# Kernel tuning notes

Measured on AMD Instinct MI355X. Metric: run time of the kernel, lower is better.

## Reference

```python
import jax, jax.numpy as jnp
from jax import lax
import numpy as np

D_MODEL = 1024
D_STATE = 16
D_CONV = 4
EXPAND = 2
D_INNER = EXPAND * D_MODEL  # 2048
DT_RANK = D_MODEL // 16     # 64
EPS = 1e-5


def _ln(x, g, b):
    mu = jnp.mean(x, axis=-1, keepdims=True)
    var = jnp.mean(jnp.square(x - mu), axis=-1, keepdims=True)
    return (x - mu) * lax.rsqrt(var + EPS) * g + b


def setup_inputs() -> dict:
    key = jax.random.key(0)
    ks = jax.random.split(key, 16)
    B, L = 2, 1024
    s = 0.02  # weight init scale
    inp = {
        'x': jax.random.normal(ks[0], (B, L, D_MODEL), jnp.float32),
        'n1_g': jnp.ones((D_MODEL,), jnp.float32),
        'n1_b': jnp.zeros((D_MODEL,), jnp.float32),
        'n2_g': jnp.ones((D_MODEL,), jnp.float32),
        'n2_b': jnp.zeros((D_MODEL,), jnp.float32),
        'in_proj_w': jax.random.normal(ks[1], (2 * D_INNER, D_MODEL), jnp.float32) * s,
        'conv_w': jax.random.normal(ks[2], (D_INNER, 1, D_CONV), jnp.float32) * 0.1,
        'conv_b': jnp.zeros((D_INNER,), jnp.float32),
        'x_proj_w': jax.random.normal(ks[3], (DT_RANK + 2 * D_STATE, D_INNER), jnp.float32) * s,
        'dt_w': jax.random.normal(ks[4], (D_INNER, DT_RANK), jnp.float32) * s,
        'dt_b': jnp.full((D_INNER,), -4.0, jnp.float32) + jax.random.normal(ks[5], (D_INNER,), jnp.float32) * 0.1,
        'A_log': jnp.tile(jnp.log(jnp.arange(1, D_STATE + 1, dtype=jnp.float32))[None, :], (D_INNER, 1)),
        'D': jnp.ones((D_INNER,), jnp.float32),
        'out_w': jax.random.normal(ks[6], (D_MODEL, D_INNER), jnp.float32) * s,
        'ffg_w': jax.random.normal(ks[7], (2 * D_MODEL, D_MODEL), jnp.float32) * s,
        'ffg_b': jnp.zeros((2 * D_MODEL,), jnp.float32),
        'ffp_w': jax.random.normal(ks[8], (D_MODEL, D_MODEL), jnp.float32) * s,
        'ffp_b': jnp.zeros((D_MODEL,), jnp.float32),
    }
    return inp


def _mamba(u, in_proj_w, conv_w, conv_b, x_proj_w, dt_w, dt_b, A_log, D, out_w):
    Bsz, L, _ = u.shape
    xz = u @ in_proj_w.T                      # [B,L,2*Di]
    x_in, z = jnp.split(xz, 2, axis=-1)
    # depthwise causal conv over time
    xc = x_in.transpose(0, 2, 1)              # [B,Di,L]
    xc = lax.conv_general_dilated(
        xc, conv_w, window_strides=(1,), padding=[(D_CONV - 1, 0)],
        dimension_numbers=('NCH', 'OIH', 'NCH'), feature_group_count=D_INNER)
    xc = jax.nn.silu(xc + conv_b[None, :, None]).transpose(0, 2, 1)  # [B,L,Di]
    # input-dependent SSM params
    x_dbl = xc @ x_proj_w.T                   # [B,L,dt_rank+2*N]
    dt, Bm, Cm = jnp.split(x_dbl, [DT_RANK, DT_RANK + D_STATE], axis=-1)
    delta = jax.nn.softplus(dt @ dt_w.T + dt_b)        # [B,L,Di]
    A = -jnp.exp(A_log)                                # [Di,N]
    dA = jnp.exp(jnp.einsum('bld,dn->bldn', delta, A))   # [B,L,Di,N]
    dBu = jnp.einsum('bld,bln,bld->bldn', delta, Bm, xc)  # [B,L,Di,N]

    def step(h, inp):
        dA_t, dBu_t, C_t = inp
        h = dA_t * h + dBu_t                  # [B,Di,N]
        y = jnp.einsum('bdn,bn->bd', h, C_t)
        return h, y

    h0 = jnp.zeros((Bsz, D_INNER, D_STATE), u.dtype)
    _, ys = lax.scan(step, h0, (dA.transpose(1, 0, 2, 3),
                                dBu.transpose(1, 0, 2, 3),
                                Cm.transpose(1, 0, 2)))
    y = ys.transpose(1, 0, 2) + xc * D        # skip via D
    y = y * jax.nn.silu(z)                    # output gate
    return y @ out_w.T


def reference(x, n1_g, n1_b, n2_g, n2_b, in_proj_w, conv_w, conv_b, x_proj_w,
              dt_w, dt_b, A_log, D, out_w, ffg_w, ffg_b, ffp_w, ffp_b):
    # x = x + ssm(norm1(x))
    x = x + _mamba(_ln(x, n1_g, n1_b), in_proj_w, conv_w, conv_b, x_proj_w,
                   dt_w, dt_b, A_log, D, out_w)
    # gated FFN residual
    normed = _ln(x, n2_g, n2_b)
    gate, val = jnp.split(normed @ ffg_w.T + ffg_b, 2, axis=-1)
    x = x + (jax.nn.silu(gate) * val) @ ffp_w.T + ffp_b
    return x
```

## Files before the change

kernel.cpp:

```cpp
#include <hip/hip_runtime.h>
#include <hip/hip_bf16.h>

#define DM 1024
#define DI 2048
#define LSEQ 1024
#define BSZ 2
#define NROWS (BSZ*LSEQ)
#define NC 32
#define CL 32

typedef __attribute__((ext_vector_type(4))) float f32x4;
typedef __attribute__((ext_vector_type(8))) short bf16x8;
typedef __hip_bfloat16 bf16;

__device__ __forceinline__ float sigmoidf_(float x){ return 1.f/(1.f+__expf(-x)); }

__global__ void cvt_kernel(const float* __restrict__ src, bf16* __restrict__ dst,
                           long n, int cols, int src_stride, int src_rows)
{
  long i = (long)blockIdx.x*blockDim.x + threadIdx.x;
  if (i >= n) return;
  int r = (int)(i / cols);
  int c = (int)(i - (long)r*cols);
  float v = (r < src_rows) ? src[(long)r*src_stride + c] : 0.f;
  dst[i] = __float2bfloat16(v);
}

__global__ __launch_bounds__(256) void ln_kernel(const float* __restrict__ x,
    const float* __restrict__ g, const float* __restrict__ b, bf16* __restrict__ out)
{
  int row = blockIdx.x;
  float4 v = ((const float4*)(x + (long)row*DM))[threadIdx.x];
  float s  = v.x+v.y+v.z+v.w;
  float s2 = v.x*v.x+v.y*v.y+v.z*v.z+v.w*v.w;
  #pragma unroll
  for (int m=32;m;m>>=1){ s += __shfl_xor(s,m); s2 += __shfl_xor(s2,m); }
  __shared__ float ws0[4], ws1[4];
  int wv = threadIdx.x>>6;
  if ((threadIdx.x&63)==0){ ws0[wv]=s; ws1[wv]=s2; }
  __syncthreads();
  s  = ws0[0]+ws0[1]+ws0[2]+ws0[3];
  s2 = ws1[0]+ws1[1]+ws1[2]+ws1[3];
  float mu  = s*(1.f/DM);
  float var = s2*(1.f/DM) - mu*mu;
  float rs  = rsqrtf(var + 1e-5f);
  int c = threadIdx.x*4;
  float4 gg = ((const float4*)g)[threadIdx.x];
  float4 bb = ((const float4*)b)[threadIdx.x];
  bf16* o = out + (long)row*DM + c;
  o[0] = __float2bfloat16((v.x-mu)*rs*gg.x + bb.x);
  o[1] = __float2bfloat16((v.y-mu)*rs*gg.y + bb.y);
  o[2] = __float2bfloat16((v.z-mu)*rs*gg.z + bb.z);
  o[3] = __float2bfloat16((v.w-mu)*rs*gg.w + bb.w);
}

template<int ACT>
__global__ __launch_bounds__(256)
void gemm_k(const short* __restrict__ A, int lda, const short* __restrict__ B, int ldb,
            int K, int Nreal, int ldo, int pstride,
            const float* __restrict__ bias, const float* __restrict__ res,
            float* __restrict__ outf, bf16* __restrict__ outb)
{
  A += (size_t)blockIdx.z * K;
  B += (size_t)blockIdx.z * K;
  if (outf) outf += (size_t)blockIdx.z * pstride;

  __shared__ short As[2][128*32];
  __shared__ short Bs[2][128*32];
  const int tid  = threadIdx.x;
  const int wave = tid>>6, lane = tid&63;
  const int m0 = blockIdx.x*128, n0 = blockIdx.y*128;
  const int wm = (wave>>1)*64, wn = (wave&1)*64;
  const int lr = lane&15, lk = lane>>4;

  f32x4 acc[4][4];
  #pragma unroll
  for (int i=0;i<4;i++)
    #pragma unroll
    for (int j=0;j<4;j++) acc[i][j] = f32x4{0.f,0.f,0.f,0.f};

  const int r0 = tid>>2;
  const int kb = (tid&3)*8;
  const short* Arow = A + (size_t)(m0+r0)*lda + kb;
  const short* Brow = B + (size_t)(n0+r0)*ldb + kb;

#define STAGE_T(buf, kt) do { \
    __builtin_amdgcn_global_load_lds((const __attribute__((address_space(1))) void*)(Arow + (kt)), \
        (__attribute__((address_space(3))) void*)(&As[buf][r0*32+kb]), 16, 0, 0); \
    __builtin_amdgcn_global_load_lds((const __attribute__((address_space(1))) void*)(Arow + (size_t)64*lda + (kt)), \
        (__attribute__((address_space(3))) void*)(&As[buf][(r0+64)*32+kb]), 16, 0, 0); \
    __builtin_amdgcn_global_load_lds((const __attribute__((address_space(1))) void*)(Brow + (kt)), \
        (__attribute__((address_space(3))) void*)(&Bs[buf][r0*32+kb]), 16, 0, 0); \
    __builtin_amdgcn_global_load_lds((const __attribute__((address_space(1))) void*)(Brow + (size_t)64*ldb + (kt)), \
        (__attribute__((address_space(3))) void*)(&Bs[buf][(r0+64)*32+kb]), 16, 0, 0); \
  } while(0)

  STAGE_T(0, 0);
  asm volatile("s_waitcnt vmcnt(0)");
  __syncthreads();
  int cur = 0;
  for (int kt = 32; kt <= K; kt += 32) {
    if (kt < K) STAGE_T(cur^1, kt);
    bf16x8 af[4], bfr[4];
    #pragma unroll
    for (int i=0;i<4;i++) af[i]  = *(const bf16x8*)(&As[cur][(wm+i*16+lr)*32 + lk*8]);
    #pragma unroll
    for (int j=0;j<4;j++) bfr[j] = *(const bf16x8*)(&Bs[cur][(wn+j*16+lr)*32 + lk*8]);
    #pragma unroll
    for (int i=0;i<4;i++)
      #pragma unroll
      for (int j=0;j<4;j++)
        acc[i][j] = __builtin_amdgcn_mfma_f32_16x16x32_bf16(af[i], bfr[j], acc[i][j], 0,0,0);
    asm volatile("s_waitcnt vmcnt(0)");
    __syncthreads();
    cur ^= 1;
  }
#undef STAGE_T

  #pragma unroll
  for (int i=0;i<4;i++){
    #pragma unroll
    for (int j=0;j<4;j++){
      int col = n0 + wn + j*16 + lr;
      if (col >= Nreal) continue;
      #pragma unroll
      for (int r=0;r<4;r++){
        int row = m0 + wm + i*16 + lk*4 + r;
        float v = acc[i][j][r];
        if (bias) v += bias[col];
        if (ACT==1){
          float ev = __expf(v);
          v = (v > 20.f) ? v : __logf(1.f + ev);
        }
        if (res)  v += res[(size_t)row*ldo + col];
        if (outf) outf[(size_t)row*ldo + col] = v;
        if (outb) outb[(size_t)row*ldo + col] = __float2bfloat16(v);
      }
    }
  }
}

__global__ __launch_bounds__(256) void red2_kernel(
    const float* __restrict__ p0, const float* __restrict__ p1,
    const float* __restrict__ bias, const float* __restrict__ res,
    float* __restrict__ outf)
{
  long i = ((long)blockIdx.x*256 + threadIdx.x)*4;
  float4 a = *(const float4*)(p0+i);
  float4 b = *(const float4*)(p1+i);
  float4 o = {a.x+b.x, a.y+b.y, a.z+b.z, a.w+b.w};
  if (bias){
    const float4 bb = *(const float4*)(bias + (int)(i & (DM-1)));
    o.x+=bb.x; o.y+=bb.y; o.z+=bb.z; o.w+=bb.w;
  }
  if (res){
    float4 r = *(const float4*)(res+i);
    o.x+=r.x; o.y+=r.y; o.z+=r.z; o.w+=r.w;
  }
  *(float4*)(outf+i) = o;
}

__global__ __launch_bounds__(256) void xproj_reduce(const float* __restrict__ part,
    float* __restrict__ xdbl, bf16* __restrict__ dt16)
{
  int i = blockIdx.x*256 + threadIdx.x;
  if (i >= NROWS*96) return;
  float s = 0.f;
  #pragma unroll
  for (int k=0;k<8;k++) s += part[(long)k*(NROWS*96) + i];
  xdbl[i] = s;
  int r = i/96, c = i - r*96;
  if (c < 64) dt16[r*64 + c] = __float2bfloat16(s);
}

__global__ __launch_bounds__(256) void conv_kernel(const bf16* __restrict__ xz,
    const float* __restrict__ w, const float* __restrict__ cb,
    float* __restrict__ xcf, bf16* __restrict__ xcb)
{
  long i = (long)blockIdx.x*blockDim.x + threadIdx.x;
  int d  = (int)(i & (DI-1));
  int bl = (int)(i >> 11);
  int l  = bl & (LSEQ-1);
  int b  = bl >> 10;
  float acc = cb[d];
  #pragma unroll
  for (int k=0;k<4;k++){
    int ls = l-3+k;
    if (ls >= 0)
      acc += __bfloat162float(xz[(long)(b*LSEQ+ls)*(2*DI) + d]) * w[d*4+k];
  }
  float s = acc * sigmoidf_(acc);
  xcf[i] = s;
  xcb[i] = __float2bfloat16(s);
}


#define H16(du, duxv, B0,B1,B2,B3) \
  h0  = __expf((du)*An0 )*h0  + (duxv)*(B0).x; \
  h1  = __expf((du)*An1 )*h1  + (duxv)*(B0).y; \
  h2  = __expf((du)*An2 )*h2  + (duxv)*(B0).z; \
  h3  = __expf((du)*An3 )*h3  + (duxv)*(B0).w; \
  h4  = __expf((du)*An4 )*h4  + (duxv)*(B1).x; \
  h5  = __expf((du)*An5 )*h5  + (duxv)*(B1).y; \
  h6  = __expf((du)*An6 )*h6  + (duxv)*(B1).z; \
  h7  = __expf((du)*An7 )*h7  + (duxv)*(B1).w; \
  h8  = __expf((du)*An8 )*h8  + (duxv)*(B2).x; \
  h9  = __expf((du)*An9 )*h9  + (duxv)*(B2).y; \
  h10 = __expf((du)*An10)*h10 + (duxv)*(B2).z; \
  h11 = __expf((du)*An11)*h11 + (duxv)*(B2).w; \
  h12 = __expf((du)*An12)*h12 + (duxv)*(B3).x; \
  h13 = __expf((du)*An13)*h13 + (duxv)*(B3).y; \
  h14 = __expf((du)*An14)*h14 + (duxv)*(B3).z; \
  h15 = __expf((du)*An15)*h15 + (duxv)*(B3).w;

#define DECL_AN(Alog_ptr, d) \
  float4 al0 = ((const float4*)((Alog_ptr) + (d)*16))[0]; \
  float4 al1 = ((const float4*)((Alog_ptr) + (d)*16))[1]; \
  float4 al2 = ((const float4*)((Alog_ptr) + (d)*16))[2]; \
  float4 al3 = ((const float4*)((Alog_ptr) + (d)*16))[3]; \
  float An0=-__expf(al0.x), An1=-__expf(al0.y), An2 =-__expf(al0.z), An3 =-__expf(al0.w); \
  float An4=-__expf(al1.x), An5=-__expf(al1.y), An6 =-__expf(al1.z), An7 =-__expf(al1.w); \
  float An8=-__expf(al2.x), An9=-__expf(al2.y), An10=-__expf(al2.z), An11=-__expf(al2.w); \
  float An12=-__expf(al3.x),An13=-__expf(al3.y),An14=-__expf(al3.z), An15=-__expf(al3.w);

__global__ __launch_bounds__(256) void scan_p1(
    const float* __restrict__ delta, const float* __restrict__ xc,
    const float* __restrict__ xdbl, const float* __restrict__ A_log,
    float* __restrict__ S, float* __restrict__ sumDu)
{
  const int tid = threadIdx.x;
  const int d   = blockIdx.x*256 + tid;
  const int c   = blockIdx.y, b = blockIdx.z;
  const int bd  = b*2048 + d;
  DECL_AN(A_log, d);
  __shared__ float sB[CL][16];
  {
    int e = tid*2;
    int r = e>>4, n = e&15;
    long row = (long)b*LSEQ + c*CL + r;
    sB[r][n]   = xdbl[row*96 + 64 + n];
    sB[r][n+1] = xdbl[row*96 + 64 + n+1];
  }
  __syncthreads();
  float h0=0,h1=0,h2=0,h3=0,h4=0,h5=0,h6=0,h7=0,
        h8=0,h9=0,h10=0,h11=0,h12=0,h13=0,h14=0,h15=0;
  float sdu = 0.f;
  const long rbase = (long)b*LSEQ + c*CL;
  #pragma unroll
  for (int s0=0; s0<CL; s0+=8){
    float du8[8], xv8[8];
    #pragma unroll
    for (int i=0;i<8;i++){
      long row = rbase + s0 + i;
      du8[i] = delta[row*DI + d];
      xv8[i] = xc[row*DI + d];
    }
    #pragma unroll
    for (int i=0;i<8;i++){
      float du = du8[i], duxv = du*xv8[i];
      sdu += du;
      const float4* bb = (const float4*)sB[s0+i];
      float4 B0=bb[0], B1=bb[1], B2=bb[2], B3=bb[3];
      H16(du, duxv, B0,B1,B2,B3);
    }
  }
  sumDu[c*4096 + bd] = sdu;
  float hs[16] = {h0,h1,h2,h3,h4,h5,h6,h7,h8,h9,h10,h11,h12,h13,h14,h15};
  #pragma unroll
  for (int n=0;n<16;n++) S[(c*16+n)*4096 + bd] = hs[n];
}

__global__ __launch_bounds__(256) void scan_p2(const float* __restrict__ S,
    const float* __restrict__ sumDu, const float* __restrict__ A_log,
    float* __restrict__ hin)
{
  int t = blockIdx.x*256 + threadIdx.x;
  int n = t >> 12, bd = t & 4095;
  int d = bd & 2047;
  float Aneg = -__expf(A_log[d*16 + n]);
  float h = 0.f;
  #pragma unroll
  for (int c=0;c<NC;c++){
    hin[(c*16+n)*4096 + bd] = h;
    float P = __expf(Aneg * sumDu[c*4096 + bd]);
    h = S[(c*16+n)*4096 + bd] + P*h;
  }
}

__global__ __launch_bounds__(256) void scan_p3(
    const float* __restrict__ delta, const float* __restrict__ xc,
    const float* __restrict__ xdbl, const bf16* __restrict__ xz,
    const float* __restrict__ A_log, const float* __restrict__ Dp,
    const float* __restrict__ hin, bf16* __restrict__ y)
{
  const int tid = threadIdx.x;
  const int d   = blockIdx.x*256 + tid;
  const int c   = blockIdx.y, b = blockIdx.z;
  const int bd  = b*2048 + d;
  DECL_AN(A_log, d);
  const float Dd = Dp[d];
  __shared__ float sB[CL][16], sC[CL][16];
  {
    int e = tid*2;
    int r = e>>4, n = e&15;
    long row = (long)b*LSEQ + c*CL + r;
    sB[r][n]   = xdbl[row*96 + 64 + n];
    sB[r][n+1] = xdbl[row*96 + 64 + n+1];
    sC[r][n]   = xdbl[row*96 + 80 + n];
    sC[r][n+1] = xdbl[row*96 + 80 + n+1];
  }
  __syncthreads();
  float h0,h1,h2,h3,h4,h5,h6,h7,h8,h9,h10,h11,h12,h13,h14,h15;
  {
    const float* hp = hin + c*16*4096 + bd;
    h0 =hp[0];       h1 =hp[4096];    h2 =hp[2*4096];  h3 =hp[3*4096];
    h4 =hp[4*4096];  h5 =hp[5*4096];  h6 =hp[6*4096];  h7 =hp[7*4096];
    h8 =hp[8*4096];  h9 =hp[9*4096];  h10=hp[10*4096]; h11=hp[11*4096];
    h12=hp[12*4096]; h13=hp[13*4096]; h14=hp[14*4096]; h15=hp[15*4096];
  }
  const long rbase = (long)b*LSEQ + c*CL;
  #pragma unroll
  for (int s0=0; s0<CL; s0+=8){
    float du8[8], xv8[8], zv8[8];
    #pragma unroll
    for (int i=0;i<8;i++){
      long row = rbase + s0 + i;
      du8[i] = delta[row*DI + d];
      xv8[i] = xc[row*DI + d];
      zv8[i] = __bfloat162float(xz[row*(2*DI) + DI + d]);
    }
    #pragma unroll
    for (int i=0;i<8;i++){
      float du = du8[i], xv = xv8[i], duxv = du*xv;
      const float4* bb = (const float4*)sB[s0+i];
      float4 B0=bb[0], B1=bb[1], B2=bb[2], B3=bb[3];
      H16(du, duxv, B0,B1,B2,B3);
      const float4* cc = (const float4*)sC[s0+i];
      float4 C0=cc[0], C1=cc[1], C2=cc[2], C3=cc[3];
      float r0 = h0*C0.x + h4*C1.x + h8 *C2.x + h12*C3.x;
      float r1 = h1*C0.y + h5*C1.y + h9 *C2.y + h13*C3.y;
      float r2 = h2*C0.z + h6*C1.z + h10*C2.z + h14*C3.z;
      float r3 = h3*C0.w + h7*C1.w + h11*C2.w + h15*C3.w;
      float r = (r0+r1) + (r2+r3) + xv*Dd;
      float z = zv8[i];
      y[(rbase+s0+i)*DI + d] = __float2bfloat16(r * (z*sigmoidf_(z)));
    }
  }
}

__global__ __launch_bounds__(256) void gated_kernel(const float* __restrict__ gv,
                                                    bf16* __restrict__ g)
{
  long i = (long)blockIdx.x*blockDim.x + threadIdx.x;
  int r = (int)(i >> 10);
  int c = (int)(i & (DM-1));
  float gt = gv[(long)r*(2*DM) + c];
  float vl = gv[(long)r*(2*DM) + DM + c];
  g[i] = __float2bfloat16(gt * sigmoidf_(gt) * vl);
}

extern "C" void kernel_launch(void* const* d_in, const int* in_sizes, int n_in,
                              void* d_out, int out_size, void* d_ws, size_t ws_size,
                              hipStream_t stream)
{
  const float* x        = (const float*)d_in[0];
  const float* n1_g     = (const float*)d_in[1];
  const float* n1_b     = (const float*)d_in[2];
  const float* n2_g     = (const float*)d_in[3];
  const float* n2_b     = (const float*)d_in[4];
  const float* in_proj_w= (const float*)d_in[5];
  const float* conv_w   = (const float*)d_in[6];
  const float* conv_b   = (const float*)d_in[7];
  const float* x_proj_w = (const float*)d_in[8];
  const float* dt_w     = (const float*)d_in[9];
  const float* dt_b     = (const float*)d_in[10];
  const float* A_log    = (const float*)d_in[11];
  const float* Dp       = (const float*)d_in[12];
  const float* out_w    = (const float*)d_in[13];
  const float* ffg_w    = (const float*)d_in[14];
  const float* ffg_b    = (const float*)d_in[15];
  const float* ffp_w    = (const float*)d_in[16];
  const float* ffp_b    = (const float*)d_in[17];

  char* ws = (char*)d_ws;
  bf16* w_inproj = (bf16*)(ws + 0);
  bf16* w_xproj  = (bf16*)(ws + 8388608);
  bf16* w_dt     = (bf16*)(ws + 8912896);
  bf16* w_out    = (bf16*)(ws + 9175040);
  bf16* w_ffg    = (bf16*)(ws + 13369344);
  bf16* w_ffp    = (bf16*)(ws + 17563648);
  bf16* x1_b     = (bf16*)(ws + 19660800);
  bf16* xz_b     = (bf16*)(ws + 23855104);
  float* part_fp = (float*)(ws + 23855104);
  bf16* xc_b     = (bf16*)(ws + 40632320);
  float* S_buf   = (float*)(ws + 40632320);
  float* sumDu   = (float*)(ws + 8388608);
  bf16* dt16     = (bf16*)(ws + 49020928);
  bf16* y_b      = (bf16*)(ws + 49283072);
  float* xc_f    = (float*)(ws + 57671680);
  float* xdbl_f  = (float*)(ws + 74448896);
  float* delta_f = (float*)(ws + 75235328);
  float* part_xp = (float*)(ws + 75235328);
  float* part_op = (float*)(ws + 75235328);
  float* x2_f    = (float*)(ws + 92012544);
  float* hin     = (float*)(ws + 92012544);
  float* outp    = (float*)d_out;

  #define GRID1(n) dim3((int)(((n)+255)/256))
  cvt_kernel<<<GRID1(4096L*1024), 256, 0, stream>>>(in_proj_w, w_inproj, 4096L*1024, 1024, 1024, 4096);
  cvt_kernel<<<GRID1(128L*2048), 256, 0, stream>>>(x_proj_w,  w_xproj,  128L*2048, 2048, 2048, 96);
  cvt_kernel<<<GRID1(2048L*64),  256, 0, stream>>>(dt_w,      w_dt,     2048L*64,   64,   64, 2048);
  cvt_kernel<<<GRID1(1024L*2048),256, 0, stream>>>(out_w,     w_out,    1024L*2048, 2048, 2048, 1024);
  cvt_kernel<<<GRID1(2048L*1024),256, 0, stream>>>(ffg_w,     w_ffg,    2048L*1024, 1024, 1024, 2048);
  cvt_kernel<<<GRID1(1024L*1024),256, 0, stream>>>(ffp_w,     w_ffp,    1024L*1024, 1024, 1024, 1024);

  ln_kernel<<<NROWS, 256, 0, stream>>>(x, n1_g, n1_b, x1_b);
  gemm_k<0><<<dim3(16,32), 256, 0, stream>>>((const short*)x1_b, 1024, (const short*)w_inproj, 1024,
      1024, 4096, 4096, 0, nullptr, nullptr, nullptr, xz_b);
  conv_kernel<<<GRID1((long)NROWS*DI), 256, 0, stream>>>(xz_b, conv_w, conv_b, xc_f, xc_b);
  gemm_k<0><<<dim3(16,1,8), 256, 0, stream>>>((const short*)xc_b, 2048, (const short*)w_xproj, 2048,
      256, 96, 96, NROWS*96, nullptr, nullptr, part_xp, nullptr);
  xproj_reduce<<<GRID1((long)NROWS*96), 256, 0, stream>>>(part_xp, xdbl_f, dt16);
  gemm_k<1><<<dim3(16,16), 256, 0, stream>>>((const short*)dt16, 64, (const short*)w_dt, 64,
      64, 2048, 2048, 0, dt_b, nullptr, delta_f, nullptr);
  scan_p1<<<dim3(8,NC,2), 256, 0, stream>>>(delta_f, xc_f, xdbl_f, A_log, S_buf, sumDu);
  scan_p2<<<dim3(256), 256, 0, stream>>>(S_buf, sumDu, A_log, hin);
  scan_p3<<<dim3(8,NC,2), 256, 0, stream>>>(delta_f, xc_f, xdbl_f, xz_b, A_log, Dp, hin, y_b);
  gemm_k<0><<<dim3(16,8,2), 256, 0, stream>>>((const short*)y_b, 2048, (const short*)w_out, 2048,
      1024, 1024, 1024, NROWS*DM, nullptr, nullptr, part_op, nullptr);
  red2_kernel<<<dim3(2048), 256, 0, stream>>>(part_op, part_op + (long)NROWS*DM, nullptr, x, x2_f);
  ln_kernel<<<NROWS, 256, 0, stream>>>(x2_f, n2_g, n2_b, x1_b);
  gemm_k<0><<<dim3(16,16), 256, 0, stream>>>((const short*)x1_b, 1024, (const short*)w_ffg, 1024,
      1024, 2048, 2048, 0, ffg_b, nullptr, delta_f, nullptr);
  gated_kernel<<<GRID1((long)NROWS*DM), 256, 0, stream>>>(delta_f, y_b);
  gemm_k<0><<<dim3(16,8,2), 256, 0, stream>>>((const short*)y_b, 1024, (const short*)w_ffp, 1024,
      512, 1024, 1024, NROWS*DM, nullptr, nullptr, part_fp, nullptr);
  red2_kernel<<<dim3(2048), 256, 0, stream>>>(part_fp, part_fp + (long)NROWS*DM, ffp_b, x2_f, outp);
  #undef GRID1
}
```

Before: 375.0 us.

## Deepen GEMM LDS pipeline to four stages and fuse weight conversions

```diff
diff --git a/kernel.cpp b/kernel.cpp
--- a/kernel.cpp
+++ b/kernel.cpp
@@ -11,19 +11,44 @@
 
 typedef __attribute__((ext_vector_type(4))) float f32x4;
 typedef __attribute__((ext_vector_type(8))) short bf16x8;
+typedef __attribute__((ext_vector_type(4))) short s16x4;
 typedef __hip_bfloat16 bf16;
 
 __device__ __forceinline__ float sigmoidf_(float x){ return 1.f/(1.f+__expf(-x)); }
-
-__global__ void cvt_kernel(const float* __restrict__ src, bf16* __restrict__ dst,
-                           long n, int cols, int src_stride, int src_rows)
-{
-  long i = (long)blockIdx.x*blockDim.x + threadIdx.x;
-  if (i >= n) return;
-  int r = (int)(i / cols);
-  int c = (int)(i - (long)r*cols);
-  float v = (r < src_rows) ? src[(long)r*src_stride + c] : 0.f;
-  dst[i] = __float2bfloat16(v);
+__device__ __forceinline__ short bfbits(float x){ bf16 h=__float2bfloat16(x); return *reinterpret_cast<short*>(&h); }
+
+#define U0 1048576L
+#define U1 (U0+65536L)
+#define U2 (U1+32768L)
+#define U3 (U2+524288L)
+#define U4 (U3+524288L)
+#define U5 (U4+262144L)
+__global__ __launch_bounds__(256) void cvt_all(
+    const float* __restrict__ s0, const float* __restrict__ s1, const float* __restrict__ s2,
+    const float* __restrict__ s3, const float* __restrict__ s4, const float* __restrict__ s5,
+    bf16* __restrict__ d0, bf16* __restrict__ d1, bf16* __restrict__ d2,
+    bf16* __restrict__ d3, bf16* __restrict__ d4, bf16* __restrict__ d5)
+{
+  long u = (long)blockIdx.x*256 + threadIdx.x;
+  if (u >= U5) return;
+  const float* src; bf16* dst; long e;
+  if (u < U0)      { src=s0; dst=d0; e=u*4; }
+  else if (u < U1) {
+    long v=u-U0; e=v*4; long row=e>>11;
+    s16x4 o;
+    if (row < 96){
+      float4 x = *(const float4*)(s1 + e);
+      o[0]=bfbits(x.x); o[1]=bfbits(x.y); o[2]=bfbits(x.z); o[3]=bfbits(x.w);
+    } else { o[0]=o[1]=o[2]=o[3]=0; }
+    *(s16x4*)(d1+e) = o; return;
+  }
+  else if (u < U2) { src=s2; dst=d2; e=(u-U1)*4; }
+  else if (u < U3) { src=s3; dst=d3; e=(u-U2)*4; }
+  else if (u < U4) { src=s4; dst=d4; e=(u-U3)*4; }
+  else             { src=s5; dst=d5; e=(u-U4)*4; }
+  float4 x = *(const float4*)(src + e);
+  s16x4 o; o[0]=bfbits(x.x); o[1]=bfbits(x.y); o[2]=bfbits(x.z); o[3]=bfbits(x.w);
+  *(s16x4*)(dst+e) = o;
 }
 
 __global__ __launch_bounds__(256) void ln_kernel(const float* __restrict__ x,
@@ -65,8 +90,8 @@
   B += (size_t)blockIdx.z * K;
   if (outf) outf += (size_t)blockIdx.z * pstride;
 
-  __shared__ short As[2][128*32];
-  __shared__ short Bs[2][128*32];
+  __shared__ short As[4][128*32];
+  __shared__ short Bs[4][128*32];
   const int tid  = threadIdx.x;
   const int wave = tid>>6, lane = tid&63;
   const int m0 = blockIdx.x*128, n0 = blockIdx.y*128;
@@ -95,12 +120,17 @@
         (__attribute__((address_space(3))) void*)(&Bs[buf][(r0+64)*32+kb]), 16, 0, 0); \
   } while(0)
 
-  STAGE_T(0, 0);
-  asm volatile("s_waitcnt vmcnt(0)");
-  __syncthreads();
-  int cur = 0;
-  for (int kt = 32; kt <= K; kt += 32) {
-    if (kt < K) STAGE_T(cur^1, kt);
+  const int nt = K >> 5;
+  {
+    const int pre = nt < 3 ? nt : 3;
+    for (int s=0; s<pre; ++s) STAGE_T(s, s*32);
+  }
+  for (int t=0; t<nt; ++t) {
+    if (t <= nt-3)      asm volatile("s_waitcnt vmcnt(8)");
+    else if (t == nt-2) asm volatile("s_waitcnt vmcnt(4)");
+    else                asm volatile("s_waitcnt vmcnt(0)");
+    __syncthreads();
+    const int cur = t & 3;
     bf16x8 af[4], bfr[4];
     #pragma unroll
     for (int i=0;i<4;i++) af[i]  = *(const bf16x8*)(&As[cur][(wm+i*16+lr)*32 + lk*8]);
@@ -111,9 +141,7 @@
       #pragma unroll
       for (int j=0;j<4;j++)
         acc[i][j] = __builtin_amdgcn_mfma_f32_16x16x32_bf16(af[i], bfr[j], acc[i][j], 0,0,0);
-    asm volatile("s_waitcnt vmcnt(0)");
-    __syncthreads();
-    cur ^= 1;
+    if (t+3 < nt) STAGE_T((t+3)&3, (t+3)*32);
   }
 #undef STAGE_T
 
@@ -193,7 +221,6 @@
   xcf[i] = s;
   xcb[i] = __float2bfloat16(s);
 }
-
 
 #define H16(du, duxv, B0,B1,B2,B3) \
   h0  = __expf((du)*An0 )*h0  + (duxv)*(B0).x; \
@@ -407,12 +434,8 @@
   float* outp    = (float*)d_out;
 
   #define GRID1(n) dim3((int)(((n)+255)/256))
-  cvt_kernel<<<GRID1(4096L*1024), 256, 0, stream>>>(in_proj_w, w_inproj, 4096L*1024, 1024, 1024, 4096);
-  cvt_kernel<<<GRID1(128L*2048), 256, 0, stream>>>(x_proj_w,  w_xproj,  128L*2048, 2048, 2048, 96);
-  cvt_kernel<<<GRID1(2048L*64),  256, 0, stream>>>(dt_w,      w_dt,     2048L*64,   64,   64, 2048);
-  cvt_kernel<<<GRID1(1024L*2048),256, 0, stream>>>(out_w,     w_out,    1024L*2048, 2048, 2048, 1024);
-  cvt_kernel<<<GRID1(2048L*1024),256, 0, stream>>>(ffg_w,     w_ffg,    2048L*1024, 1024, 1024, 2048);
-  cvt_kernel<<<GRID1(1024L*1024),256, 0, stream>>>(ffp_w,     w_ffp,    1024L*1024, 1024, 1024, 1024);
+  cvt_all<<<dim3(9600), 256, 0, stream>>>(in_proj_w, x_proj_w, dt_w, out_w, ffg_w, ffp_w,
+                                          w_inproj, w_xproj, w_dt, w_out, w_ffg, w_ffp);
 
   ln_kernel<<<NROWS, 256, 0, stream>>>(x, n1_g, n1_b, x1_b);
   gemm_k<0><<<dim3(16,32), 256, 0, stream>>>((const short*)x1_b, 1024, (const short*)w_inproj, 1024,
```

Result: faster. 348.1 us (-7.2%).
